# Optimization experiments

Hardware: AMD Instinct MI355X
Metric: run time of the kernel (lower is better)

Reference implementation:

```python
import jax, jax.numpy as jnp
import numpy as np

J, T, N_VARS, K = 64, 64, 4, 8   # n_inputs, terms per input poly, vars, Bernstein coeffs per var
I = 64                            # layer_size (output nodes)


def setup_inputs() -> dict:
    key = jax.random.key(0)
    k1, k2, k3, k4, k5, k6 = jax.random.split(key, 6)
    return {
        "layer_inputs_under": jax.random.normal(k1, (J, T, N_VARS, K), jnp.float32),
        "layer_inputs_over": jax.random.normal(k2, (J, T, N_VARS, K), jnp.float32),
        "layer_inputs_under_degrees": jax.random.randint(k3, (J, N_VARS), 0, 5).astype(jnp.float32),
        "layer_inputs_over_degrees": jax.random.randint(k4, (J, N_VARS), 0, 5).astype(jnp.float32),
        "layer_weights": jax.random.normal(k5, (I, J), jnp.float32),
        "layer_biases": jax.random.normal(k6, (I,), jnp.float32),
    }


def _scale_polys(polys, w):
    """mult_with_constant, vectorized over nodes and inputs.
    In IBF a polynomial is scaled by a constant by scaling the FIRST variable's
    coefficient row of every term.  polys: [J,T,n,k], w: [I,J] -> [I,J,T,n,k]."""
    i = w.shape[0]
    row0 = polys[None, :, :, 0:1, :] * w[:, :, None, None, None]        # [I,J,T,1,k]
    rest = jnp.broadcast_to(polys[None, :, :, 1:, :],
                            (i, polys.shape[0], polys.shape[1], polys.shape[2] - 1, polys.shape[3]))
    return jnp.concatenate([row0, rest], axis=3)


def _layer(liu, lio, w, b):
    """LayerModule.forward with activation='linear' (identity path of NodeModule).
    node_under = sum_j (w_neg[i,j]*over_j + w_pos[i,j]*under_j) + bias term
    node_over  = sum_j (w_pos[i,j]*over_j + w_neg[i,j]*under_j) + bias term
    sum_2_polys == concatenation of term lists; add_with_constant appends one
    constant term (row0 = bias, remaining variable rows = ones)."""
    w_pos = jax.nn.relu(w)
    w_neg = -jax.nn.relu(-w)
    j, t, n, k = liu.shape
    i = w.shape[0]

    def combine(wa, wb):
        pa = _scale_polys(lio, wa).reshape(i, j * t, n, k)  # scaled over-polys
        pb = _scale_polys(liu, wb).reshape(i, j * t, n, k)  # scaled under-polys
        return jnp.concatenate([pa, pb], axis=1)            # [I, 2JT, n, k]

    under = combine(w_neg, w_pos)
    over = combine(w_pos, w_neg)

    bias_term = jnp.concatenate(
        [b[:, None, None, None] * jnp.ones((i, 1, 1, k), b.dtype),
         jnp.ones((i, 1, n - 1, k), b.dtype)], axis=2)      # [I,1,n,k]
    under = jnp.concatenate([under, bias_term], axis=1)     # [I, 2JT+1, n, k]
    over = jnp.concatenate([over, bias_term], axis=1)
    return under, over


def reference(layer_inputs_under, layer_inputs_over, layer_inputs_under_degrees,
              layer_inputs_over_degrees, layer_weights, layer_biases):
    under, over = _layer(layer_inputs_under, layer_inputs_over, layer_weights, layer_biases)
    # degree of each node poly = elementwise max of contributing input degrees
    deg = jnp.maximum(layer_inputs_under_degrees, layer_inputs_over_degrees).max(axis=0)  # [n]
    i = layer_weights.shape[0]
    under_deg = jnp.broadcast_to(deg, (i, deg.shape[0]))
    over_deg = under_deg
    return under, over, under_deg, over_deg
```

## Files before the change

### kernel.cpp

```cpp
#include <hip/hip_runtime.h>

namespace {
constexpr int Jc = 64, Tc = 64, NVc = 4, Ic = 64;
constexpr int F4_TERM  = 8;
constexpr int TERMS    = 2 * Jc * Tc + 1;
constexpr int NODE_F4  = TERMS * F4_TERM;
constexpr int TILE_F4  = Tc * F4_TERM;
constexpr long long SIDE_F4 = (long long)Ic * NODE_F4;
constexpr long long DEG_BASE_FLT = 2LL * SIDE_F4 * 4;
constexpr int SPANS   = 16;
constexpr int SPAN_F4 = (2 * Tc * Jc / SPANS) * F4_TERM;
constexpr int MAIN_BLOCKS = 2 * Ic * SPANS;
}

typedef float v4f __attribute__((ext_vector_type(4)));

__device__ __forceinline__ void store4(float4* p, float x, float y, float z, float w) {
    v4f v = {x, y, z, w};
    *reinterpret_cast<v4f*>(p) = v;
}

__global__ __launch_bounds__(256) void layer_kernel(
    const float4* __restrict__ liu,
    const float4* __restrict__ lio,
    const float*  __restrict__ ud,
    const float*  __restrict__ od,
    const float*  __restrict__ w,
    const float*  __restrict__ bias,
    float*        __restrict__ outf)
{
    float4* out = reinterpret_cast<float4*>(outf);
    const int b   = blockIdx.x;
    const int tid = (int)threadIdx.x;

    if (b < MAIN_BLOCKS) {
        const int p = b & (SPANS - 1);
        const int i = (b >> 4) & 63;
        const int s = b >> 10;

        float sv[8];
        const float4* srcs[8];
        #pragma unroll
        for (int ts = 0; ts < 8; ++ts) {
            const int jj = p * 8 + ts;
            const int h  = jj >> 6;
            const int j  = jj & 63;
            const float wv = w[i * Jc + j];
            const float wp = fmaxf(wv, 0.0f);
            const float wn = fminf(wv, 0.0f);
            sv[ts]   = (h == s) ? wn : wp;
            srcs[ts] = (h ? liu : lio) + j * TILE_F4;
        }

        const bool isv0 = (tid & 7) < 2;

        float4* dst = out + (long long)s * SIDE_F4 + (long long)i * NODE_F4
                          + p * SPAN_F4;
        #pragma unroll
        for (int r = 0; r < 16; ++r) {
            const int f  = r * 256 + tid;
            const int ts = r >> 1;
            const float4 v = srcs[ts][f & 511];
            const float sc = isv0 ? sv[ts] : 1.0f;
            store4(dst + f, v.x * sc, v.y * sc, v.z * sc, v.w * sc);
        }
    } else {
        #pragma unroll
        for (int r = 0; r < 4; ++r) {
            const int t    = r * 256 + tid;
            const int reg  = t >> 3;
            const int i    = reg >> 1;
            const int s    = reg & 1;
            const int sub  = t & 7;
            const float val = (sub < 2) ? bias[i] : 1.0f;
            const long long off = (long long)s * SIDE_F4 + (long long)i * NODE_F4
                                  + (long long)(2 * Jc * Tc) * F4_TERM + sub;
            store4(out + off, val, val, val, val);
        }
        const int lane = tid & 63;
        float m[NVc];
        #pragma unroll
        for (int v = 0; v < NVc; ++v)
            m[v] = fmaxf(ud[lane * NVc + v], od[lane * NVc + v]);
        #pragma unroll
        for (int mask = 1; mask < 64; mask <<= 1) {
            #pragma unroll
            for (int v = 0; v < NVc; ++v)
                m[v] = fmaxf(m[v], __shfl_xor(m[v], mask, 64));
        }
        const float dv = m[tid & 3];
        outf[DEG_BASE_FLT + tid] = dv;
        outf[DEG_BASE_FLT + 256 + tid] = dv;
    }
}

extern "C" void kernel_launch(void* const* d_in, const int* in_sizes, int n_in,
                              void* d_out, int out_size, void* d_ws, size_t ws_size,
                              hipStream_t stream) {
    const float4* liu  = (const float4*)d_in[0];
    const float4* lio  = (const float4*)d_in[1];
    const float*  ud   = (const float*)d_in[2];
    const float*  od   = (const float*)d_in[3];
    const float*  w    = (const float*)d_in[4];
    const float*  bias = (const float*)d_in[5];
    float* outf = (float*)d_out;

    layer_kernel<<<dim3(MAIN_BLOCKS + 1), dim3(256), 0, stream>>>(
        liu, lio, ud, od, w, bias, outf);
}
```

Measured before the change: 144.4 us.

## Load each input float4 once and reuse it across sixteen output regions

The work mapping changes so each thread loads one input float4 and writes it, scaled, into 16 different (side, node) output regions. Before, each block streamed a contiguous span of one region and re-read inputs that every region shares. The aim is to cut input reads from L2 per output and raise the ratio of stores to loads in this write-bound copy-scale kernel. In exchange, each thread's 16 stores are spread across distant regions, and it makes 16 scattered weight loads instead of 8 per block.

```diff
diff --git a/kernel.cpp b/kernel.cpp
--- a/kernel.cpp
+++ b/kernel.cpp
@@ -5,12 +5,11 @@
 constexpr int F4_TERM  = 8;
 constexpr int TERMS    = 2 * Jc * Tc + 1;
 constexpr int NODE_F4  = TERMS * F4_TERM;
+constexpr int REG_F4   = 2 * Jc * Tc * F4_TERM;
 constexpr int TILE_F4  = Tc * F4_TERM;
 constexpr long long SIDE_F4 = (long long)Ic * NODE_F4;
 constexpr long long DEG_BASE_FLT = 2LL * SIDE_F4 * 4;
-constexpr int SPANS   = 16;
-constexpr int SPAN_F4 = (2 * Tc * Jc / SPANS) * F4_TERM;
-constexpr int MAIN_BLOCKS = 2 * Ic * SPANS;
+constexpr int MAIN_BLOCKS = 2048;
 }
 
 typedef float v4f __attribute__((ext_vector_type(4)));
@@ -34,35 +33,28 @@
     const int tid = (int)threadIdx.x;
 
     if (b < MAIN_BLOCKS) {
-        const int p = b & (SPANS - 1);
-        const int i = (b >> 4) & 63;
-        const int s = b >> 10;
+        const int breg = b >> 8;
+        const int m    = ((b & 255) << 8) + tid;
+        const int jj   = m >> 9;
+        const int f4i  = m & 511;
+        const int h    = jj >> 6;
+        const int j    = jj & 63;
 
-        float sv[8];
-        const float4* srcs[8];
+        const float4 va = ((h ? liu : lio) + j * TILE_F4)[f4i];
+        const bool isv0 = (f4i & 7) < 2;
+
         #pragma unroll
-        for (int ts = 0; ts < 8; ++ts) {
-            const int jj = p * 8 + ts;
-            const int h  = jj >> 6;
-            const int j  = jj & 63;
+        for (int r = 0; r < 16; ++r) {
+            const int region = r * 8 + breg;
+            const int s = region >> 6;
+            const int i = region & 63;
             const float wv = w[i * Jc + j];
             const float wp = fmaxf(wv, 0.0f);
             const float wn = fminf(wv, 0.0f);
-            sv[ts]   = (h == s) ? wn : wp;
-            srcs[ts] = (h ? liu : lio) + j * TILE_F4;
-        }
-
-        const bool isv0 = (tid & 7) < 2;
-
-        float4* dst = out + (long long)s * SIDE_F4 + (long long)i * NODE_F4
-                          + p * SPAN_F4;
-        #pragma unroll
-        for (int r = 0; r < 16; ++r) {
-            const int f  = r * 256 + tid;
-            const int ts = r >> 1;
-            const float4 v = srcs[ts][f & 511];
-            const float sc = isv0 ? sv[ts] : 1.0f;
-            store4(dst + f, v.x * sc, v.y * sc, v.z * sc, v.w * sc);
+            const float sc0 = (h == s) ? wn : wp;
+            const float sc  = isv0 ? sc0 : 1.0f;
+            float4* dst = out + (long long)region * NODE_F4 + m;
+            store4(dst, va.x * sc, va.y * sc, va.z * sc, va.w * sc);
         }
     } else {
         #pragma unroll
@@ -74,21 +66,21 @@
             const int sub  = t & 7;
             const float val = (sub < 2) ? bias[i] : 1.0f;
             const long long off = (long long)s * SIDE_F4 + (long long)i * NODE_F4
-                                  + (long long)(2 * Jc * Tc) * F4_TERM + sub;
+                                  + (long long)REG_F4 + sub;
             store4(out + off, val, val, val, val);
         }
         const int lane = tid & 63;
-        float m[NVc];
+        float mx[NVc];
         #pragma unroll
         for (int v = 0; v < NVc; ++v)
-            m[v] = fmaxf(ud[lane * NVc + v], od[lane * NVc + v]);
+            mx[v] = fmaxf(ud[lane * NVc + v], od[lane * NVc + v]);
         #pragma unroll
         for (int mask = 1; mask < 64; mask <<= 1) {
             #pragma unroll
             for (int v = 0; v < NVc; ++v)
-                m[v] = fmaxf(m[v], __shfl_xor(m[v], mask, 64));
+                mx[v] = fmaxf(mx[v], __shfl_xor(mx[v], mask, 64));
         }
-        const float dv = m[tid & 3];
+        const float dv = mx[tid & 3];
         outf[DEG_BASE_FLT + tid] = dv;
         outf[DEG_BASE_FLT + 256 + tid] = dv;
     }
```

Result: no change. 142.3 us (-1.5%).
